# Kernel tuning notes

Hardware: AMD Instinct MI355X
Metric: run time of the kernel (lower is better)

Reference implementation:

```python
import jax, jax.numpy as jnp
import numpy as np
import math

D_MODEL = 1024
NUM_HEADS = 16
D_K = 64
B, T = 2, 2048


def setup_inputs() -> dict:
    key = jax.random.key(0)
    ks = jax.random.split(key, 12)
    s = 0.02
    return {
        "Q": jax.random.normal(ks[0], (B, T, D_MODEL), jnp.float32),
        "K": jax.random.normal(ks[1], (B, T, D_MODEL), jnp.float32),
        "V": jax.random.normal(ks[2], (B, T, D_MODEL), jnp.float32),
        # stacked per-head projection weights: [H, d_model, d_k]
        "Wq": jax.random.normal(ks[3], (NUM_HEADS, D_MODEL, D_K), jnp.float32) * s,
        "bq": jax.random.normal(ks[4], (NUM_HEADS, D_K), jnp.float32) * s,
        "Wk": jax.random.normal(ks[5], (NUM_HEADS, D_MODEL, D_K), jnp.float32) * s,
        "bk": jax.random.normal(ks[6], (NUM_HEADS, D_K), jnp.float32) * s,
        "Wv": jax.random.normal(ks[7], (NUM_HEADS, D_MODEL, D_K), jnp.float32) * s,
        "bv": jax.random.normal(ks[8], (NUM_HEADS, D_K), jnp.float32) * s,
        "Wo": jax.random.normal(ks[9], (D_MODEL, D_MODEL), jnp.float32) * s,
        "bo": jax.random.normal(ks[10], (D_MODEL,), jnp.float32) * s,
    }


def reference(Q, K, V, Wq, bq, Wk, bk, Wv, bv, Wo, bo):
    scale = 1.0 / math.sqrt(D_K)
    # fused batched per-head projections (replaces the Python per-head loop)
    Qh = jnp.einsum("btd,hdk->bhtk", Q, Wq) + bq[None, :, None, :]
    Kh = jnp.einsum("btd,hdk->bhtk", K, Wk) + bk[None, :, None, :]
    Vh = jnp.einsum("btd,hdk->bhtk", V, Wv) + bv[None, :, None, :]
    scores = jnp.einsum("bhtk,bhsk->bhts", Qh, Kh) * scale  # [B,H,T,T]
    attn = jax.nn.softmax(scores, axis=-1)
    ctx = jnp.einsum("bhts,bhsk->bhtk", attn, Vh)  # [B,H,T,d_k]
    # Faithful to the original: plain view of contiguous [B,H,T,d] into
    # [B,T,H*d] WITHOUT transposing head/time (matches torch .view semantics).
    bsz, nt = Q.shape[0], Q.shape[1]
    x = ctx.reshape(bsz, nt, NUM_HEADS * D_K)
    out = x @ Wo.T + bo
    # dropout with p=0.0 is identity; omitted for determinism
    return out
```

## Files before the change

### kernel.cpp

```cpp
#include <hip/hip_runtime.h>
#include <stdint.h>

typedef __attribute__((ext_vector_type(8))) short short8;
typedef __attribute__((ext_vector_type(4))) short short4v;
typedef __attribute__((ext_vector_type(4))) float float4v;

#define MFMA16(a, b, c) __builtin_amdgcn_mfma_f32_16x16x32_bf16((a), (b), (c), 0, 0, 0)

__device__ __forceinline__ ushort f2bf_rne(float f) {
  union { float f; unsigned u; } x; x.f = f;
  unsigned r = x.u + 0x7FFFu + ((x.u >> 16) & 1u);
  return (ushort)(r >> 16);
}
__device__ __forceinline__ ushort f2bf_trunc(float f) {
  union { float f; unsigned u; } x; x.f = f;
  return (ushort)(x.u >> 16);
}
__device__ __forceinline__ void gload16(const ushort* g, ushort* lds) {
  __builtin_amdgcn_global_load_lds(
      (__attribute__((address_space(1))) unsigned int*)g,
      (__attribute__((address_space(3))) unsigned int*)lds, 16, 0, 0);
}

#define CEXP 0.1803368801111204f

__device__ __forceinline__ void transpose64f(const float* __restrict__ in, int is,
                                             ushort* __restrict__ out, int os,
                                             ushort* lds ) {
  const int t = threadIdx.x;
#pragma unroll
  for (int it = 0; it < 2; ++it) {
    int e = it * 2048 + t * 8;
    int r = e >> 6, c = e & 63;
    const float* p = in + (size_t)r * is + c;
    float4 x0 = *(const float4*)p;
    float4 x1 = *(const float4*)(p + 4);
    ushort tv[8] __attribute__((aligned(16))) = {
        f2bf_rne(x0.x), f2bf_rne(x0.y), f2bf_rne(x0.z), f2bf_rne(x0.w),
        f2bf_rne(x1.x), f2bf_rne(x1.y), f2bf_rne(x1.z), f2bf_rne(x1.w)};
    *(uint4*)&lds[r * 72 + c] = *(const uint4*)tv;
  }
  __syncthreads();
  const int cc = t >> 2;
  const int rg = (t & 3) * 16;
  ushort tmp[16] __attribute__((aligned(16)));
#pragma unroll
  for (int i = 0; i < 16; ++i) tmp[i] = lds[(rg + i) * 72 + cc];
  *(uint4*)&out[(size_t)cc * os + rg] = *(const uint4*)&tmp[0];
  *(uint4*)&out[(size_t)cc * os + rg + 8] = *(const uint4*)&tmp[8];
}

__global__ __launch_bounds__(256) void prep_kernel(
    const float* __restrict__ Q, const float* __restrict__ K,
    const float* __restrict__ V, const float* __restrict__ Wo,
    const float* __restrict__ Wq, const float* __restrict__ Wk,
    const float* __restrict__ Wv, ushort* __restrict__ Qb, ushort* __restrict__ Kb,
    ushort* __restrict__ Vb, ushort* __restrict__ WoB, ushort* __restrict__ BtQ,
    ushort* __restrict__ BtK, ushort* __restrict__ BtV) {
  __shared__ ushort lds[64 * 72];
  const int bx = blockIdx.x;
  if (bx < 6656) {
    const float* s;
    ushort* d;
    int i;
    if (bx < 6144) {
      const int plane = bx >> 11;
      s = plane == 0 ? Q : (plane == 1 ? K : V);
      d = plane == 0 ? Qb : (plane == 1 ? Kb : Vb);
      i = ((bx & 2047) * 256 + threadIdx.x) * 8;
    } else {
      s = Wo;
      d = WoB;
      i = ((bx - 6144) * 256 + threadIdx.x) * 8;
    }
    float4 a = *(const float4*)(s + i);
    float4 b = *(const float4*)(s + i + 4);
    ushort t[8] __attribute__((aligned(16))) = {
        f2bf_rne(a.x), f2bf_rne(a.y), f2bf_rne(a.z), f2bf_rne(a.w),
        f2bf_rne(b.x), f2bf_rne(b.y), f2bf_rne(b.z), f2bf_rne(b.w)};
    *(uint4*)(d + i) = *(const uint4*)t;
  } else {
    const int rb = bx - 6656;
    const int dt = rb & 15, h = (rb >> 4) & 15, z = rb >> 8;
    const float* W = z == 0 ? Wq : (z == 1 ? Wk : Wv);
    ushort* Bt = z == 0 ? BtQ : (z == 1 ? BtK : BtV);
    transpose64f(W + h * 65536 + dt * 4096, 64, Bt + h * 65536 + dt * 64, 1024, lds);
  }
}

__global__ __launch_bounds__(256, 2) void repack_w_kernel(
    const float* __restrict__ Wq, const float* __restrict__ Wk,
    const float* __restrict__ Wv, ushort* __restrict__ BtQ, ushort* __restrict__ BtK,
    ushort* __restrict__ BtV) {
  __shared__ ushort lds[64 * 72];
  const float* W = blockIdx.z == 0 ? Wq : (blockIdx.z == 1 ? Wk : Wv);
  ushort* Bt = blockIdx.z == 0 ? BtQ : (blockIdx.z == 1 ? BtK : BtV);
  const int h = blockIdx.y, dt = blockIdx.x;
  transpose64f(W + h * 65536 + dt * 4096, 64, Bt + h * 65536 + dt * 64, 1024, lds);
}

template <int F32>
__device__ __forceinline__ void stage16(const void* G, size_t eoff, ushort* ldst) {
  if (F32) {
    const float* p = (const float*)G + eoff;
    float4 x0 = *(const float4*)p;
    float4 x1 = *(const float4*)(p + 4);
    ushort t[8] __attribute__((aligned(16))) = {
        f2bf_rne(x0.x), f2bf_rne(x0.y), f2bf_rne(x0.z), f2bf_rne(x0.w),
        f2bf_rne(x1.x), f2bf_rne(x1.y), f2bf_rne(x1.z), f2bf_rne(x1.w)};
    *(uint4*)ldst = *(const uint4*)t;
  } else {
    gload16((const ushort*)G + eoff, ldst);
  }
}

template <int AF32, int BF32>
__device__ __forceinline__ void gemm_body_basic(const void* __restrict__ A,
                                                const void* __restrict__ Bt,
                                                const float* __restrict__ bias,
                                                void* __restrict__ C, int cmode,
                                                float ascale, int N, int K, ushort* lA,
                                                ushort* lB) {
  const int tid = threadIdx.x;
  const int l = tid & 63, lane15 = l & 15, quad = l >> 4;
  const int mbase = blockIdx.y * 128, nbase = blockIdx.x * 128;
  const int w = tid >> 6;
  const int wrow = (w >> 1) * 64, wcol = (w & 1) * 64;
  const int e0 = tid * 8;
  const int e1 = 2048 + tid * 8;
  const int r0 = e0 >> 5, c0 = e0 & 31;
  const int r1 = e1 >> 5, c1 = e1 & 31;

  float4v acc[4][4];
#pragma unroll
  for (int i = 0; i < 4; ++i)
#pragma unroll
    for (int j = 0; j < 4; ++j) acc[i][j] = (float4v){0.f, 0.f, 0.f, 0.f};

  for (int kb = 0; kb < K; kb += 32) {
    __syncthreads();
    stage16<AF32>(A, (size_t)(mbase + r0) * K + c0 + kb, &lA[e0]);
    stage16<AF32>(A, (size_t)(mbase + r1) * K + c1 + kb, &lA[e1]);
    stage16<BF32>(Bt, (size_t)(nbase + r0) * K + c0 + kb, &lB[e0]);
    stage16<BF32>(Bt, (size_t)(nbase + r1) * K + c1 + kb, &lB[e1]);
    asm volatile("s_waitcnt vmcnt(0)" ::: "memory");
    __syncthreads();
    short8 a[4], b[4];
#pragma unroll
    for (int i = 0; i < 4; ++i) {
      a[i] = *(const short8*)&lA[(wrow + i * 16 + lane15) * 32 + quad * 8];
      b[i] = *(const short8*)&lB[(wcol + i * 16 + lane15) * 32 + quad * 8];
    }
#pragma unroll
    for (int i = 0; i < 4; ++i)
#pragma unroll
      for (int j = 0; j < 4; ++j) acc[i][j] = MFMA16(a[i], b[j], acc[i][j]);
  }

  if (cmode == 3) {
    __syncthreads();
    uint* sp = (uint*)lA + w * 576;
    const int bb = mbase >> 11;
    const int tb = (mbase & 2047) + wrow;
#pragma unroll
    for (int j = 0; j < 4; ++j) {
      {
        const int n = nbase + wcol + j * 16 + lane15;
        const float bvs = bias[n];
#pragma unroll
        for (int i = 0; i < 4; ++i)
#pragma unroll
          for (int rp = 0; rp < 2; ++rp) {
            const uint lo = f2bf_rne((acc[i][j][2 * rp] + bvs) * ascale);
            const uint hi = f2bf_rne((acc[i][j][2 * rp + 1] + bvs) * ascale);
            sp[36 * lane15 + i * 8 + quad * 2 + rp] = lo | (hi << 16);
          }
      }
#pragma unroll
      for (int t = 0; t < 2; ++t) {
        const int row = t * 8 + (l >> 3);
        const int c = l & 7;
        uint4 d = *(const uint4*)(sp + 36 * row + 4 * c);
        const int ng = nbase + wcol + j * 16 + row;
        ushort* dst = (ushort*)C + ((size_t)(bb * 1024 + ng)) * 2048 + tb + c * 8;
        *(uint4*)dst = d;
      }
    }
    return;
  }

#pragma unroll
  for (int j = 0; j < 4; ++j) {
    const int n = nbase + wcol + j * 16 + lane15;
    const float bvs = bias[n];
#pragma unroll
    for (int i = 0; i < 4; ++i) {
      const int m0 = mbase + wrow + i * 16 + quad * 4;
#pragma unroll
      for (int r = 0; r < 4; ++r) {
        const float val = (acc[i][j][r] + bvs) * ascale;
        if (cmode == 1) {
          const int m = m0 + r;
          const int bb = m >> 11, t = m & 2047;
          ((ushort*)C)[((size_t)(bb * 1024 + n)) * 2048 + t] = f2bf_rne(val);
        } else if (cmode == 2) {
          ((float*)C)[(size_t)(m0 + r) * N + n] = val;
        } else {
          ((ushort*)C)[(size_t)(m0 + r) * N + n] = f2bf_rne(val);
        }
      }
    }
  }
}

__global__ __launch_bounds__(256, 2) void proj3_kernel(
    const ushort* __restrict__ Qb, const ushort* __restrict__ Kb,
    const ushort* __restrict__ Vb, const ushort* __restrict__ BtQ,
    const ushort* __restrict__ BtK, const ushort* __restrict__ BtV,
    const float* __restrict__ bq, const float* __restrict__ bk,
    const float* __restrict__ bv, ushort* __restrict__ Qh, ushort* __restrict__ Kh,
    ushort* __restrict__ Vt) {
  __shared__ ushort lA[5120], lB[4096];
  if (blockIdx.z == 0)
    gemm_body_basic<0, 0>(Qb, BtQ, bq, Qh, 0, CEXP, 1024, 1024, lA, lB);
  else if (blockIdx.z == 1)
    gemm_body_basic<0, 0>(Kb, BtK, bk, Kh, 0, 1.0f, 1024, 1024, lA, lB);
  else
    gemm_body_basic<0, 0>(Vb, BtV, bv, Vt, 3, 1.0f, 1024, 1024, lA, lB);
}

__global__ __launch_bounds__(256, 2) void gemm_out_kernel(
    const ushort* __restrict__ X, const ushort* __restrict__ WoB,
    const float* __restrict__ bo, float* __restrict__ out) {
  __shared__ ushort lA[4096], lB[2048];
  const int tid = threadIdx.x;
  const int l = tid & 63, lane15 = l & 15, quad = l >> 4;
  const int mbase = blockIdx.y * 128, nbase = blockIdx.x * 64;
  const int wv = tid >> 6;
  const int wrow = wv * 32;
  const int e0 = tid * 8;
  const int e1 = 2048 + tid * 8;
  const int r0 = e0 >> 5, c0 = e0 & 31;
  const int r1 = e1 >> 5, c1 = e1 & 31;
  const ushort* Ag0 = X + (size_t)(mbase + r0) * 1024 + c0;
  const ushort* Ag1 = X + (size_t)(mbase + r1) * 1024 + c1;
  const ushort* Bg0 = WoB + (size_t)(nbase + r0) * 1024 + c0;

  float4v acc[2][4];
#pragma unroll
  for (int i = 0; i < 2; ++i)
#pragma unroll
    for (int j = 0; j < 4; ++j) acc[i][j] = (float4v){0.f, 0.f, 0.f, 0.f};

  for (int kb = 0; kb < 1024; kb += 32) {
    __syncthreads();
    gload16(Ag0 + kb, &lA[e0]);
    gload16(Ag1 + kb, &lA[e1]);
    gload16(Bg0 + kb, &lB[e0]);
    asm volatile("s_waitcnt vmcnt(0)" ::: "memory");
    __syncthreads();
    short8 a[2], b[4];
#pragma unroll
    for (int i = 0; i < 2; ++i)
      a[i] = *(const short8*)&lA[(wrow + i * 16 + lane15) * 32 + quad * 8];
#pragma unroll
    for (int j = 0; j < 4; ++j)
      b[j] = *(const short8*)&lB[(j * 16 + lane15) * 32 + quad * 8];
#pragma unroll
    for (int i = 0; i < 2; ++i)
#pragma unroll
      for (int j = 0; j < 4; ++j) acc[i][j] = MFMA16(a[i], b[j], acc[i][j]);
  }

#pragma unroll
  for (int j = 0; j < 4; ++j) {
    const int n = nbase + j * 16 + lane15;
    const float bvs = bo[n];
#pragma unroll
    for (int i = 0; i < 2; ++i) {
      const int m0 = mbase + wrow + i * 16 + quad * 4;
#pragma unroll
      for (int r = 0; r < 4; ++r) out[(size_t)(m0 + r) * 1024 + n] = acc[i][j][r] + bvs;
    }
  }
}

__global__ __launch_bounds__(256, 2) void proj3f_kernel(
    const float* __restrict__ Q, const float* __restrict__ Kin,
    const float* __restrict__ V, const ushort* __restrict__ BtQ,
    const ushort* __restrict__ BtK, const ushort* __restrict__ BtV,
    const float* __restrict__ bq, const float* __restrict__ bk,
    const float* __restrict__ bv, ushort* __restrict__ Qh, ushort* __restrict__ Kh,
    ushort* __restrict__ Vt) {
  __shared__ ushort lA[5120], lB[4096];
  if (blockIdx.z == 0)
    gemm_body_basic<1, 0>(Q, BtQ, bq, Qh, 0, CEXP, 1024, 1024, lA, lB);
  else if (blockIdx.z == 1)
    gemm_body_basic<1, 0>(Kin, BtK, bk, Kh, 0, 1.0f, 1024, 1024, lA, lB);
  else
    gemm_body_basic<1, 0>(V, BtV, bv, Vt, 3, 1.0f, 1024, 1024, lA, lB);
}

__global__ __launch_bounds__(256, 2) void gemm_btf_kernel(
    const ushort* __restrict__ X, const float* __restrict__ Wo,
    const float* __restrict__ bo, float* __restrict__ out) {
  __shared__ ushort lA[5120], lB[4096];
  gemm_body_basic<0, 1>(X, Wo, bo, out, 2, 1.0f, 1024, 1024, lA, lB);
}

__global__ __launch_bounds__(256, 4) void attn_kernel(const ushort* __restrict__ Qh,
                                                      const ushort* __restrict__ Kh,
                                                      const ushort* __restrict__ Vt,
                                                      ushort* __restrict__ ctxout) {
  __shared__ ushort lK[2][64 * 64];
  __shared__ ushort lV[2][64 * 64];
  const int tid = threadIdx.x, l = tid & 63, wv = tid >> 6;
  const int lane15 = l & 15, quad = l >> 4;
  const int bh = blockIdx.x, b = bh >> 4, h = bh & 15;
  const int q0 = blockIdx.y * 64 + wv * 16;

  const int sr = tid >> 3;
  const int scb = (tid & 7) ^ (sr & 7);
  const ushort* Kp = Kh + (size_t)(b * 2048) * 1024 + h * 64;
  const ushort* Vp = Vt + (size_t)(bh * 64) * 2048;
  const ushort* Kg0 = Kp + (size_t)sr * 1024 + scb * 8;
  const ushort* Kg1 = Kp + (size_t)(sr + 32) * 1024 + scb * 8;
  const ushort* Vg0 = Vp + (size_t)sr * 2048 + scb * 8;
  const ushort* Vg1 = Vp + (size_t)(sr + 32) * 2048 + scb * 8;

  const ushort* qrow = Qh + (size_t)(b * 2048 + q0 + lane15) * 1024 + h * 64;
  const short8 qa0 = *(const short8*)&qrow[quad * 8];
  const short8 qa1 = *(const short8*)&qrow[32 + quad * 8];

  const int xm = lane15 & 7;
  const int fr0 = lane15 * 64 + ((quad ^ xm) * 8);
  const int fr1 = lane15 * 64 + (((quad + 4) ^ xm) * 8);

  const short8 ones = {0x3F80, 0x3F80, 0x3F80, 0x3F80, 0x3F80, 0x3F80, 0x3F80, 0x3F80};

  float4v o[4];
  float4v lf = (float4v){0.f, 0.f, 0.f, 0.f};
#pragma unroll
  for (int i = 0; i < 4; ++i) o[i] = (float4v){0.f, 0.f, 0.f, 0.f};

  gload16(Kg0, &lK[0][tid * 8]);
  gload16(Kg1, &lK[0][(256 + tid) * 8]);
  gload16(Vg0, &lV[0][tid * 8]);
  gload16(Vg1, &lV[0][(256 + tid) * 8]);
  asm volatile("s_waitcnt vmcnt(0)" ::: "memory");
  __syncthreads();

  int cur = 0;
  for (int s0 = 0; s0 < 2048; s0 += 64) {
    if (s0 + 64 < 2048) {
      gload16(Kg0 + (size_t)(s0 + 64) * 1024, &lK[cur ^ 1][tid * 8]);
      gload16(Kg1 + (size_t)(s0 + 64) * 1024, &lK[cur ^ 1][(256 + tid) * 8]);
      gload16(Vg0 + (s0 + 64), &lV[cur ^ 1][tid * 8]);
      gload16(Vg1 + (s0 + 64), &lV[cur ^ 1][(256 + tid) * 8]);
    }
    const ushort* Kl = &lK[cur][0];
    const ushort* Vl = &lV[cur][0];

    float4v sb[4];
    __builtin_amdgcn_s_setprio(1);
#pragma unroll
    for (int i = 0; i < 4; ++i) {
      short8 k0 = *(const short8*)&Kl[i * 1024 + fr0];
      short8 k1 = *(const short8*)&Kl[i * 1024 + fr1];
      float4v c = (float4v){0.f, 0.f, 0.f, 0.f};
      c = MFMA16(k0, qa0, c);
      c = MFMA16(k1, qa1, c);
      sb[i] = c;
    }
    __builtin_amdgcn_s_setprio(0);

    uint wpk[4][2];
#pragma unroll
    for (int i = 0; i < 4; ++i) {
      const float e0 = __builtin_amdgcn_exp2f(sb[i][0]);
      const float e1 = __builtin_amdgcn_exp2f(sb[i][1]);
      const float e2 = __builtin_amdgcn_exp2f(sb[i][2]);
      const float e3 = __builtin_amdgcn_exp2f(sb[i][3]);
      asm("v_cvt_pk_bf16_f32 %0, %1, %2" : "=v"(wpk[i][0]) : "v"(e0), "v"(e1));
      asm("v_cvt_pk_bf16_f32 %0, %1, %2" : "=v"(wpk[i][1]) : "v"(e2), "v"(e3));
    }

    union PK { uint w[4]; short8 v; };
    PK u0, u1;
    {
      uint a0 = wpk[0][0], b0 = wpk[1][0];
      asm("v_permlane32_swap_b32 %0, %1" : "+v"(a0), "+v"(b0));
      asm("v_permlane16_swap_b32 %0, %1" : "+v"(a0), "+v"(b0));
      uint a1 = wpk[0][1], b1 = wpk[1][1];
      asm("v_permlane32_swap_b32 %0, %1" : "+v"(a1), "+v"(b1));
      asm("v_permlane16_swap_b32 %0, %1" : "+v"(a1), "+v"(b1));
      u0.w[0] = a0; u0.w[1] = a1; u0.w[2] = b0; u0.w[3] = b1;
      uint a2 = wpk[2][0], b2 = wpk[3][0];
      asm("v_permlane32_swap_b32 %0, %1" : "+v"(a2), "+v"(b2));
      asm("v_permlane16_swap_b32 %0, %1" : "+v"(a2), "+v"(b2));
      uint a3 = wpk[2][1], b3 = wpk[3][1];
      asm("v_permlane32_swap_b32 %0, %1" : "+v"(a3), "+v"(b3));
      asm("v_permlane16_swap_b32 %0, %1" : "+v"(a3), "+v"(b3));
      u1.w[0] = a2; u1.w[1] = a3; u1.w[2] = b2; u1.w[3] = b3;
    }
    const short8 pa0 = u0.v;
    const short8 pa1 = u1.v;

    __builtin_amdgcn_s_setprio(1);
    lf = MFMA16(pa0, ones, lf);
    lf = MFMA16(pa1, ones, lf);
#pragma unroll
    for (int nf = 0; nf < 4; ++nf) {
      short8 v0 = *(const short8*)&Vl[nf * 1024 + fr0];
      short8 v1 = *(const short8*)&Vl[nf * 1024 + fr1];
      o[nf] = MFMA16(pa0, v0, o[nf]);
      o[nf] = MFMA16(pa1, v1, o[nf]);
    }
    __builtin_amdgcn_s_setprio(0);

    asm volatile("s_waitcnt vmcnt(0)" ::: "memory");
    __syncthreads();
    cur ^= 1;
  }

  float inv[4];
#pragma unroll
  for (int r = 0; r < 4; ++r) inv[r] = (lf[r] > 0.f) ? 1.0f / lf[r] : 0.0f;
  ushort* crow = ctxout + ((size_t)bh * 2048 + q0) * 64;
#pragma unroll
  for (int nf = 0; nf < 4; ++nf)
#pragma unroll
    for (int r = 0; r < 4; ++r)
      crow[(size_t)(quad * 4 + r) * 64 + nf * 16 + lane15] = f2bf_rne(o[nf][r] * inv[r]);
}

extern "C" void kernel_launch(void* const* d_in, const int* in_sizes, int n_in,
                              void* d_out, int out_size, void* d_ws, size_t ws_size,
                              hipStream_t stream) {
  const float* Q = (const float*)d_in[0];
  const float* K = (const float*)d_in[1];
  const float* V = (const float*)d_in[2];
  const float* Wq = (const float*)d_in[3];
  const float* bq = (const float*)d_in[4];
  const float* Wk = (const float*)d_in[5];
  const float* bk = (const float*)d_in[6];
  const float* Wv = (const float*)d_in[7];
  const float* bv = (const float*)d_in[8];
  const float* Wo = (const float*)d_in[9];
  const float* bo = (const float*)d_in[10];
  float* out = (float*)d_out;
  ushort* ws = (ushort*)d_ws;

  if (ws_size >= (58ull << 20)) {
    ushort* Qh = ws;
    ushort* Kh = Qh + (4 << 20);
    ushort* Vt = Kh + (4 << 20);
    ushort* BtQ = Vt + (4 << 20);
    ushort* BtK = BtQ + (1 << 20);
    ushort* BtV = BtK + (1 << 20);
    ushort* X = BtQ;
    ushort* WoB = ws + (16ull << 20);
    ushort* Qb = WoB + (1 << 20);
    ushort* Kb = Qb + (4 << 20);
    ushort* Vb = Kb + (4 << 20);

    prep_kernel<<<dim3(7424), 256, 0, stream>>>(Q, K, V, Wo, Wq, Wk, Wv, Qb, Kb, Vb,
                                                WoB, BtQ, BtK, BtV);
    proj3_kernel<<<dim3(8, 32, 3), 256, 0, stream>>>(Qb, Kb, Vb, BtQ, BtK, BtV, bq, bk,
                                                     bv, Qh, Kh, Vt);
    attn_kernel<<<dim3(32, 32), 256, 0, stream>>>(Qh, Kh, Vt, X);
    gemm_out_kernel<<<dim3(16, 32), 256, 0, stream>>>(X, WoB, bo, out);
  } else {
    ushort* Qh = ws;
    ushort* Kh = Qh + (4 << 20);
    ushort* Vt = Kh + (4 << 20);
    ushort* R = Vt + (4 << 20);
    ushort* BtQ = R;
    ushort* BtK = R + (1 << 20);
    ushort* BtV = R + (2 << 20);
    ushort* X = R;

    repack_w_kernel<<<dim3(16, 16, 3), 256, 0, stream>>>(Wq, Wk, Wv, BtQ, BtK, BtV);
    proj3f_kernel<<<dim3(8, 32, 3), 256, 0, stream>>>(Q, K, V, BtQ, BtK, BtV, bq, bk, bv,
                                                      Qh, Kh, Vt);
    attn_kernel<<<dim3(32, 32), 256, 0, stream>>>(Qh, Kh, Vt, X);
    gemm_btf_kernel<<<dim3(8, 32), 256, 0, stream>>>(X, Wo, bo, out);
  }
}
```

Baseline: 219.0 us.

## Process two 16-row query blocks per wave in attention kernel

Each wave now handles 32 query rows instead of 16, so every K and V fragment read from LDS feeds two sets of MFMAs, and each block covers 128 queries. The grid is halved and the launch bound drops to 2 blocks per CU to make room for the doubled accumulator registers. This halves global K/V traffic and LDS reads per query, at the cost of lower occupancy and only 512 blocks to spread across the CUs.

```diff
diff --git a/kernel.cpp b/kernel.cpp
--- a/kernel.cpp
+++ b/kernel.cpp
@@ -308,7 +308,7 @@
   gemm_body_basic<0, 1>(X, Wo, bo, out, 2, 1.0f, 1024, 1024, lA, lB);
 }
 
-__global__ __launch_bounds__(256, 4) void attn_kernel(const ushort* __restrict__ Qh,
+__global__ __launch_bounds__(256, 2) void attn_kernel(const ushort* __restrict__ Qh,
                                                       const ushort* __restrict__ Kh,
                                                       const ushort* __restrict__ Vt,
                                                       ushort* __restrict__ ctxout) {
@@ -317,7 +317,7 @@
   const int tid = threadIdx.x, l = tid & 63, wv = tid >> 6;
   const int lane15 = l & 15, quad = l >> 4;
   const int bh = blockIdx.x, b = bh >> 4, h = bh & 15;
-  const int q0 = blockIdx.y * 64 + wv * 16;
+  const int q0 = blockIdx.y * 128 + wv * 32;
 
   const int sr = tid >> 3;
   const int scb = (tid & 7) ^ (sr & 7);
@@ -328,9 +328,12 @@
   const ushort* Vg0 = Vp + (size_t)sr * 2048 + scb * 8;
   const ushort* Vg1 = Vp + (size_t)(sr + 32) * 2048 + scb * 8;
 
-  const ushort* qrow = Qh + (size_t)(b * 2048 + q0 + lane15) * 1024 + h * 64;
-  const short8 qa0 = *(const short8*)&qrow[quad * 8];
-  const short8 qa1 = *(const short8*)&qrow[32 + quad * 8];
+  const ushort* qrow0 = Qh + (size_t)(b * 2048 + q0 + lane15) * 1024 + h * 64;
+  const ushort* qrow1 = qrow0 + 16 * 1024;
+  const short8 qa00 = *(const short8*)&qrow0[quad * 8];
+  const short8 qa01 = *(const short8*)&qrow0[32 + quad * 8];
+  const short8 qa10 = *(const short8*)&qrow1[quad * 8];
+  const short8 qa11 = *(const short8*)&qrow1[32 + quad * 8];
 
   const int xm = lane15 & 7;
   const int fr0 = lane15 * 64 + ((quad ^ xm) * 8);
@@ -338,10 +341,14 @@
 
   const short8 ones = {0x3F80, 0x3F80, 0x3F80, 0x3F80, 0x3F80, 0x3F80, 0x3F80, 0x3F80};
 
-  float4v o[4];
-  float4v lf = (float4v){0.f, 0.f, 0.f, 0.f};
-#pragma unroll
-  for (int i = 0; i < 4; ++i) o[i] = (float4v){0.f, 0.f, 0.f, 0.f};
+  float4v o[2][4];
+  float4v lf[2];
+#pragma unroll
+  for (int qb = 0; qb < 2; ++qb) {
+    lf[qb] = (float4v){0.f, 0.f, 0.f, 0.f};
+#pragma unroll
+    for (int i = 0; i < 4; ++i) o[qb][i] = (float4v){0.f, 0.f, 0.f, 0.f};
+  }
 
   gload16(Kg0, &lK[0][tid * 8]);
   gload16(Kg1, &lK[0][(256 + tid) * 8]);
@@ -361,33 +368,39 @@
     const ushort* Kl = &lK[cur][0];
     const ushort* Vl = &lV[cur][0];
 
-    float4v sb[4];
+    float4v sb0[4], sb1[4];
     __builtin_amdgcn_s_setprio(1);
 #pragma unroll
     for (int i = 0; i < 4; ++i) {
       short8 k0 = *(const short8*)&Kl[i * 1024 + fr0];
       short8 k1 = *(const short8*)&Kl[i * 1024 + fr1];
-      float4v c = (float4v){0.f, 0.f, 0.f, 0.f};
-      c = MFMA16(k0, qa0, c);
-      c = MFMA16(k1, qa1, c);
-      sb[i] = c;
+      float4v c0 = (float4v){0.f, 0.f, 0.f, 0.f};
+      c0 = MFMA16(k0, qa00, c0);
+      c0 = MFMA16(k1, qa01, c0);
+      sb0[i] = c0;
+      float4v c1 = (float4v){0.f, 0.f, 0.f, 0.f};
+      c1 = MFMA16(k0, qa10, c1);
+      c1 = MFMA16(k1, qa11, c1);
+      sb1[i] = c1;
     }
     __builtin_amdgcn_s_setprio(0);
 
-    uint wpk[4][2];
-#pragma unroll
-    for (int i = 0; i < 4; ++i) {
-      const float e0 = __builtin_amdgcn_exp2f(sb[i][0]);
-      const float e1 = __builtin_amdgcn_exp2f(sb[i][1]);
-      const float e2 = __builtin_amdgcn_exp2f(sb[i][2]);
-      const float e3 = __builtin_amdgcn_exp2f(sb[i][3]);
-      asm("v_cvt_pk_bf16_f32 %0, %1, %2" : "=v"(wpk[i][0]) : "v"(e0), "v"(e1));
-      asm("v_cvt_pk_bf16_f32 %0, %1, %2" : "=v"(wpk[i][1]) : "v"(e2), "v"(e3));
-    }
-
     union PK { uint w[4]; short8 v; };
-    PK u0, u1;
-    {
+    short8 pA0[2], pA1[2];
+#pragma unroll
+    for (int qb = 0; qb < 2; ++qb) {
+      const float4v* sb = qb == 0 ? sb0 : sb1;
+      uint wpk[4][2];
+#pragma unroll
+      for (int i = 0; i < 4; ++i) {
+        const float e0 = __builtin_amdgcn_exp2f(sb[i][0]);
+        const float e1 = __builtin_amdgcn_exp2f(sb[i][1]);
+        const float e2 = __builtin_amdgcn_exp2f(sb[i][2]);
+        const float e3 = __builtin_amdgcn_exp2f(sb[i][3]);
+        asm("v_cvt_pk_bf16_f32 %0, %1, %2" : "=v"(wpk[i][0]) : "v"(e0), "v"(e1));
+        asm("v_cvt_pk_bf16_f32 %0, %1, %2" : "=v"(wpk[i][1]) : "v"(e2), "v"(e3));
+      }
+      PK u0, u1;
       uint a0 = wpk[0][0], b0 = wpk[1][0];
       asm("v_permlane32_swap_b32 %0, %1" : "+v"(a0), "+v"(b0));
       asm("v_permlane16_swap_b32 %0, %1" : "+v"(a0), "+v"(b0));
@@ -402,19 +415,23 @@
       asm("v_permlane32_swap_b32 %0, %1" : "+v"(a3), "+v"(b3));
       asm("v_permlane16_swap_b32 %0, %1" : "+v"(a3), "+v"(b3));
       u1.w[0] = a2; u1.w[1] = a3; u1.w[2] = b2; u1.w[3] = b3;
-    }
-    const short8 pa0 = u0.v;
-    const short8 pa1 = u1.v;
+      pA0[qb] = u0.v;
+      pA1[qb] = u1.v;
+    }
 
     __builtin_amdgcn_s_setprio(1);
-    lf = MFMA16(pa0, ones, lf);
-    lf = MFMA16(pa1, ones, lf);
+    lf[0] = MFMA16(pA0[0], ones, lf[0]);
+    lf[0] = MFMA16(pA1[0], ones, lf[0]);
+    lf[1] = MFMA16(pA0[1], ones, lf[1]);
+    lf[1] = MFMA16(pA1[1], ones, lf[1]);
 #pragma unroll
     for (int nf = 0; nf < 4; ++nf) {
       short8 v0 = *(const short8*)&Vl[nf * 1024 + fr0];
       short8 v1 = *(const short8*)&Vl[nf * 1024 + fr1];
-      o[nf] = MFMA16(pa0, v0, o[nf]);
-      o[nf] = MFMA16(pa1, v1, o[nf]);
+      o[0][nf] = MFMA16(pA0[0], v0, o[0][nf]);
+      o[0][nf] = MFMA16(pA1[0], v1, o[0][nf]);
+      o[1][nf] = MFMA16(pA0[1], v0, o[1][nf]);
+      o[1][nf] = MFMA16(pA1[1], v1, o[1][nf]);
     }
     __builtin_amdgcn_s_setprio(0);
 
@@ -423,15 +440,19 @@
     cur ^= 1;
   }
 
-  float inv[4];
-#pragma unroll
-  for (int r = 0; r < 4; ++r) inv[r] = (lf[r] > 0.f) ? 1.0f / lf[r] : 0.0f;
-  ushort* crow = ctxout + ((size_t)bh * 2048 + q0) * 64;
-#pragma unroll
-  for (int nf = 0; nf < 4; ++nf)
-#pragma unroll
-    for (int r = 0; r < 4; ++r)
-      crow[(size_t)(quad * 4 + r) * 64 + nf * 16 + lane15] = f2bf_rne(o[nf][r] * inv[r]);
+#pragma unroll
+  for (int qb = 0; qb < 2; ++qb) {
+    float inv[4];
+#pragma unroll
+    for (int r = 0; r < 4; ++r) inv[r] = (lf[qb][r] > 0.f) ? 1.0f / lf[qb][r] : 0.0f;
+    ushort* crow = ctxout + ((size_t)bh * 2048 + q0 + qb * 16) * 64;
+#pragma unroll
+    for (int nf = 0; nf < 4; ++nf)
+#pragma unroll
+      for (int r = 0; r < 4; ++r)
+        crow[(size_t)(quad * 4 + r) * 64 + nf * 16 + lane15] =
+            f2bf_rne(o[qb][nf][r] * inv[r]);
+  }
 }
 
 extern "C" void kernel_launch(void* const* d_in, const int* in_sizes, int n_in,
@@ -468,7 +489,7 @@
                                                 WoB, BtQ, BtK, BtV);
     proj3_kernel<<<dim3(8, 32, 3), 256, 0, stream>>>(Qb, Kb, Vb, BtQ, BtK, BtV, bq, bk,
                                                      bv, Qh, Kh, Vt);
-    attn_kernel<<<dim3(32, 32), 256, 0, stream>>>(Qh, Kh, Vt, X);
+    attn_kernel<<<dim3(32, 16), 256, 0, stream>>>(Qh, Kh, Vt, X);
     gemm_out_kernel<<<dim3(16, 32), 256, 0, stream>>>(X, WoB, bo, out);
   } else {
     ushort* Qh = ws;
@@ -483,7 +504,7 @@
     repack_w_kernel<<<dim3(16, 16, 3), 256, 0, stream>>>(Wq, Wk, Wv, BtQ, BtK, BtV);
     proj3f_kernel<<<dim3(8, 32, 3), 256, 0, stream>>>(Q, K, V, BtQ, BtK, BtV, bq, bk, bv,
                                                       Qh, Kh, Vt);
-    attn_kernel<<<dim3(32, 32), 256, 0, stream>>>(Qh, Kh, Vt, X);
+    attn_kernel<<<dim3(32, 16), 256, 0, stream>>>(Qh, Kh, Vt, X);
     gemm_btf_kernel<<<dim3(8, 32), 256, 0, stream>>>(X, Wo, bo, out);
   }
 }
```

New measurement: 218.6 us. Within noise of the previous version (-0.2%).
